# Kernel optimization log

Measured on AMD Instinct MI355X. Metric: run time of the kernel, lower is better.

The kernel has to match this reference:

```python
import jax, jax.numpy as jnp
import numpy as np

H = 1024  # lstm_hidden_dim
E = 1024  # embedding_size
T = 512   # seq_len
B = 128   # batch


def setup_inputs() -> dict:
    key = jax.random.key(0)
    k0, k1, k2, k3 = jax.random.split(key, 4)
    bound = 1.0 / np.sqrt(H)
    embeds = jax.random.normal(k0, (T, B, E), dtype=jnp.float32)
    # Stacked gate weights in order [g, i, f, o]; same math as 8 separate GEMMs.
    W_x = jax.random.uniform(k1, (E, 4 * H), jnp.float32, -bound, bound)
    W_h = jax.random.uniform(k2, (H, 4 * H), jnp.float32, -bound, bound)
    b = jax.random.uniform(k3, (4 * H,), jnp.float32, -bound, bound)
    b = b.at[2 * H:3 * H].add(1.0)  # forget-gate bias +1
    return {"embeds": embeds, "W_x": W_x, "W_h": W_h, "b": b}


def reference(embeds, W_x, W_h, b):
    Tn, Bn, _ = embeds.shape
    # Batch all input projections into one big GEMM (same math as per-step GEMMs).
    xproj = jnp.einsum('tbe,ef->tbf', embeds, W_x) + b  # [T, B, 4H]
    h0 = jnp.zeros((Bn, H), embeds.dtype)
    c0 = jnp.zeros((Bn, H), embeds.dtype)

    def step(carry, xp):
        h, c = carry
        z = xp + h @ W_h  # [B, 4H]
        g = jnp.tanh(z[:, :H])
        i = jax.nn.sigmoid(z[:, H:2 * H])
        f = jax.nn.sigmoid(z[:, 2 * H:3 * H])
        o = jax.nn.sigmoid(z[:, 3 * H:])
        c_new = g * i + c * f
        h_new = jnp.tanh(c_new) * o
        # Original module records h BEFORE the update at step t (h_prev).
        return (h_new, c_new), h

    _, h_total = jax.lax.scan(step, (h0, c0), xproj)
    return h_total  # [T, B, H], h_total[0] is zeros
```

## Files before the change

### kernel.cpp

```cpp
#include <hip/hip_runtime.h>
#include <hip/hip_bf16.h>

typedef __attribute__((ext_vector_type(8)))  short          bf16x8;
typedef __attribute__((ext_vector_type(4)))  float          f32x4;
typedef __attribute__((ext_vector_type(8)))  unsigned short us8;

__device__ __forceinline__ unsigned short f2b(float f) {
  union { __hip_bfloat16 h; unsigned short u; } v;
  v.h = __float2bfloat16(f);
  return v.u;
}
__device__ __forceinline__ float b2f(unsigned short u) {
  union { unsigned u; float f; } v; v.u = ((unsigned)u) << 16; return v.f;
}
__device__ __forceinline__ float sigf(float x) {
  return __builtin_amdgcn_rcpf(1.f + __expf(-x));
}
__device__ __forceinline__ float tanhf_(float x) {
  return 2.f * __builtin_amdgcn_rcpf(1.f + __expf(-2.f * x)) - 1.f;
}

__global__ __launch_bounds__(256) void conv_all(const float* __restrict__ embeds,
                                                const float* __restrict__ Wx,
                                                const float* __restrict__ Wh,
                                                unsigned short* __restrict__ ebf,
                                                unsigned short* __restrict__ wxf,
                                                unsigned short* __restrict__ whp) {
  const int b = blockIdx.x;
  if (b < 32768) {
    const int id = b * 256 + threadIdx.x;
    const int l  = id & 63;
    const int kt = (id >> 6) & 31;
    const int rt = id >> 11;
    const size_t src = ((size_t)(rt * 16 + (l & 15))) * 1024 + kt * 32 + (l >> 4) * 8;
    const float4 v0 = *(const float4*)(embeds + src);
    const float4 v1 = *(const float4*)(embeds + src + 4);
    us8 o;
    o[0]=f2b(v0.x); o[1]=f2b(v0.y); o[2]=f2b(v0.z); o[3]=f2b(v0.w);
    o[4]=f2b(v1.x); o[5]=f2b(v1.y); o[6]=f2b(v1.z); o[7]=f2b(v1.w);
    *(us8*)(ebf + (size_t)id * 8) = o;
  } else if (b < 34816) {
    const int id = (b - 32768) * 256 + threadIdx.x;
    const int l  = id & 63;
    const int kt = (id >> 6) & 31;
    const int c  = id >> 11;
    const int col = c * 16 + (l & 15);
    const int k0 = kt * 32 + (l >> 4) * 8;
    us8 o;
    #pragma unroll
    for (int j = 0; j < 8; ++j) o[j] = f2b(Wx[(size_t)(k0 + j) * 4096 + col]);
    *(us8*)(wxf + (size_t)id * 8) = o;
  } else {
    const int id = (b - 34816) * 256 + threadIdx.x;
    const int l  = id & 63;
    const int kt = (id >> 6) & 7;
    const int nt = (id >> 9) & 7;
    const int kq = (id >> 12) & 3;
    const int n  = id >> 14;
    const int zi = nt * 16 + (l & 15);
    const int col = (zi >> 5) * 1024 + n * 32 + (zi & 31);
    const int k0 = kq * 256 + kt * 32 + (l >> 4) * 8;
    us8 o;
    #pragma unroll
    for (int j = 0; j < 8; ++j) o[j] = f2b(Wh[(size_t)(k0 + j) * 4096 + col]);
    *(us8*)(whp + (size_t)id * 8) = o;
  }
}

__global__ __launch_bounds__(256, 2) void gemm_xproj_reg(
    const unsigned short* __restrict__ ebf,
    const unsigned short* __restrict__ wxf,
    const float* __restrict__ bias,
    unsigned short* __restrict__ xp) {
  const int lane = threadIdx.x & 63;
  const int wv = threadIdx.x >> 6;
  const int w = blockIdx.x * 4 + wv;
  const int ct = w & 31;
  const int rt = w >> 5;

  float bvf[8];
  #pragma unroll
  for (int nt = 0; nt < 8; ++nt) bvf[nt] = bias[ct * 128 + nt * 16 + (lane & 15)];

  f32x4 acc[4][8];
  #pragma unroll
  for (int a = 0; a < 4; ++a)
    #pragma unroll
    for (int nt = 0; nt < 8; ++nt) acc[a][nt] = f32x4{0.f,0.f,0.f,0.f};

  for (int kt = 0; kt < 32; ++kt) {
    bf16x8 af[4], bfr[8];
    #pragma unroll
    for (int a = 0; a < 4; ++a)
      af[a] = *(const bf16x8*)(ebf + (size_t)((4 * rt + a) * 32 + kt) * 512 + lane * 8);
    #pragma unroll
    for (int nt = 0; nt < 8; ++nt)
      bfr[nt] = *(const bf16x8*)(wxf + (size_t)((ct * 8 + nt) * 32 + kt) * 512 + lane * 8);
    #pragma unroll
    for (int a = 0; a < 4; ++a)
      #pragma unroll
      for (int nt = 0; nt < 8; ++nt)
        acc[a][nt] = __builtin_amdgcn_mfma_f32_16x16x32_bf16(af[a], bfr[nt], acc[a][nt], 0, 0, 0);
  }

  #pragma unroll
  for (int a = 0; a < 4; ++a) {
    const int row0 = rt * 64 + a * 16 + (lane >> 4) * 4;
    #pragma unroll
    for (int nt = 0; nt < 8; ++nt) {
      const int col = ct * 128 + nt * 16 + (lane & 15);
      #pragma unroll
      for (int rr = 0; rr < 4; ++rr)
        xp[(size_t)(row0 + rr) * 4096 + col] = f2b(acc[a][nt][rr] + bvf[nt]);
    }
  }
}

__global__ __launch_bounds__(256, 1) void lstm_recur(
    const unsigned short* __restrict__ xproj,
    const unsigned short* __restrict__ Wp,
    unsigned short* __restrict__ hbuf,
    float* __restrict__ out,
    unsigned* __restrict__ flags) {
  __shared__ float zpart[10][16][132];
  const int tid = threadIdx.x;
  const int lane = tid & 63;
  const int kq = tid >> 6;
  const int m = blockIdx.x >> 5;
  const int n = blockIdx.x & 31;

  bf16x8 wf[64];
  {
    const unsigned short* wb = Wp + ((size_t)(n * 4 + kq) * 64) * 512 + lane * 8;
    #pragma unroll
    for (int f = 0; f < 64; ++f) wf[f] = *(const bf16x8*)(wb + f * 512);
  }

  const int r    = tid >> 4;
  const int hg   = tid & 15;
  const int hc0  = n * 32 + hg * 2;
  const int grow = m * 16 + r;

  float cr0 = 0.f, cr1 = 0.f;
  const size_t xbase = (size_t)grow * 4096 + hc0;
  unsigned* bcast = flags + (m * 32 + (lane & 31)) * 32 + n;
  const unsigned* myf = flags + (size_t)(m * 32 + n) * 32 + kq * 8 + (lane & 7);

  unsigned xu0, xu1, xu2, xu3;
  {
    const unsigned short* xpp = xproj + xbase;
    asm volatile("global_load_dword %0, %1, off" : "=v"(xu0) : "v"(xpp));
    asm volatile("global_load_dword %0, %1, off" : "=v"(xu1) : "v"(xpp + 1024));
    asm volatile("global_load_dword %0, %1, off" : "=v"(xu2) : "v"(xpp + 2048));
    asm volatile("global_load_dword %0, %1, off" : "=v"(xu3) : "v"(xpp + 3072));
  }

  const size_t aoff = ((size_t)(m * 16 + (lane & 15))) * 1024 + kq * 256 + (lane >> 4) * 8;

  for (int t = 0; t < 511; ++t) {
    const unsigned short* ab = hbuf + (t & 1) * 131072 + aoff;

    bf16x8 av0, av1, av2, av3, av4, av5, av6, av7;
    __builtin_amdgcn_sched_barrier(0);
    asm volatile("global_load_dwordx4 %0, %1, off sc0 sc1"            : "=v"(av0) : "v"(ab));
    asm volatile("global_load_dwordx4 %0, %1, off offset:64 sc0 sc1"  : "=v"(av1) : "v"(ab));
    asm volatile("global_load_dwordx4 %0, %1, off offset:128 sc0 sc1" : "=v"(av2) : "v"(ab));
    asm volatile("global_load_dwordx4 %0, %1, off offset:192 sc0 sc1" : "=v"(av3) : "v"(ab));
    asm volatile("global_load_dwordx4 %0, %1, off offset:256 sc0 sc1" : "=v"(av4) : "v"(ab));
    asm volatile("global_load_dwordx4 %0, %1, off offset:320 sc0 sc1" : "=v"(av5) : "v"(ab));
    asm volatile("global_load_dwordx4 %0, %1, off offset:384 sc0 sc1" : "=v"(av6) : "v"(ab));
    asm volatile("global_load_dwordx4 %0, %1, off offset:448 sc0 sc1" : "=v"(av7) : "v"(ab));
    asm volatile("s_waitcnt vmcnt(0)" ::: "memory");
    __builtin_amdgcn_sched_barrier(0);

    f32x4 ac0 = {0.f,0.f,0.f,0.f}, ac1 = {0.f,0.f,0.f,0.f};
    f32x4 ac2 = {0.f,0.f,0.f,0.f}, ac3 = {0.f,0.f,0.f,0.f};
    f32x4 ac4 = {0.f,0.f,0.f,0.f}, ac5 = {0.f,0.f,0.f,0.f};
    f32x4 ac6 = {0.f,0.f,0.f,0.f}, ac7 = {0.f,0.f,0.f,0.f};
#define MF_STEP(AV, KT) \
    ac0 = __builtin_amdgcn_mfma_f32_16x16x32_bf16(AV, wf[ 0 + KT], ac0, 0, 0, 0); \
    ac1 = __builtin_amdgcn_mfma_f32_16x16x32_bf16(AV, wf[ 8 + KT], ac1, 0, 0, 0); \
    ac2 = __builtin_amdgcn_mfma_f32_16x16x32_bf16(AV, wf[16 + KT], ac2, 0, 0, 0); \
    ac3 = __builtin_amdgcn_mfma_f32_16x16x32_bf16(AV, wf[24 + KT], ac3, 0, 0, 0); \
    ac4 = __builtin_amdgcn_mfma_f32_16x16x32_bf16(AV, wf[32 + KT], ac4, 0, 0, 0); \
    ac5 = __builtin_amdgcn_mfma_f32_16x16x32_bf16(AV, wf[40 + KT], ac5, 0, 0, 0); \
    ac6 = __builtin_amdgcn_mfma_f32_16x16x32_bf16(AV, wf[48 + KT], ac6, 0, 0, 0); \
    ac7 = __builtin_amdgcn_mfma_f32_16x16x32_bf16(AV, wf[56 + KT], ac7, 0, 0, 0);
    MF_STEP(av0, 0) MF_STEP(av1, 1) MF_STEP(av2, 2) MF_STEP(av3, 3)
    MF_STEP(av4, 4) MF_STEP(av5, 5) MF_STEP(av6, 6) MF_STEP(av7, 7)
#undef MF_STEP

    {
      const int crow = (lane >> 4) * 4, ccol = lane & 15;
#define DUMP(NT, AC) \
      zpart[kq][crow + 0][NT * 16 + ccol] = AC[0]; \
      zpart[kq][crow + 1][NT * 16 + ccol] = AC[1]; \
      zpart[kq][crow + 2][NT * 16 + ccol] = AC[2]; \
      zpart[kq][crow + 3][NT * 16 + ccol] = AC[3];
      DUMP(0, ac0) DUMP(1, ac1) DUMP(2, ac2) DUMP(3, ac3)
      DUMP(4, ac4) DUMP(5, ac5) DUMP(6, ac6) DUMP(7, ac7)
#undef DUMP
    }
    __syncthreads();

    float zc[4][2];
    #pragma unroll
    for (int g = 0; g < 4; ++g)
      #pragma unroll
      for (int j = 0; j < 2; ++j) {
        const int col = g * 32 + hg * 2 + j;
        zc[g][j] = (zpart[0][r][col] + zpart[1][r][col])
                 + (zpart[2][r][col] + zpart[3][r][col]);
      }

    float hv0, hv1;
    {
      const float zg = zc[0][0] + b2f((unsigned short)(xu0 & 0xffffu));
      const float zi = zc[1][0] + b2f((unsigned short)(xu1 & 0xffffu));
      const float zf = zc[2][0] + b2f((unsigned short)(xu2 & 0xffffu));
      const float zo = zc[3][0] + b2f((unsigned short)(xu3 & 0xffffu));
      cr0 = tanhf_(zg) * sigf(zi) + cr0 * sigf(zf);
      hv0 = tanhf_(cr0) * sigf(zo);
    }
    {
      const float zg = zc[0][1] + b2f((unsigned short)(xu0 >> 16));
      const float zi = zc[1][1] + b2f((unsigned short)(xu1 >> 16));
      const float zf = zc[2][1] + b2f((unsigned short)(xu2 >> 16));
      const float zo = zc[3][1] + b2f((unsigned short)(xu3 >> 16));
      cr1 = tanhf_(zg) * sigf(zi) + cr1 * sigf(zf);
      hv1 = tanhf_(cr1) * sigf(zo);
    }

    if (t < 510) {
      const unsigned hp = (unsigned)f2b(hv0) | ((unsigned)f2b(hv1) << 16);
      unsigned short* hd = hbuf + ((t & 1) ^ 1) * 131072 + (size_t)grow * 1024 + hc0;
      asm volatile("global_store_dword %0, %1, off sc0 sc1" :: "v"(hd), "v"(hp) : "memory");
      asm volatile("s_waitcnt vmcnt(0)" ::: "memory");
      __syncthreads();
      if (kq == 0 && lane < 32) {
        const unsigned g1 = (unsigned)(t + 1);
        asm volatile("global_store_dword %0, %1, off sc0 sc1" :: "v"(bcast), "v"(g1) : "memory");
      }
    }

    float2 ho; ho.x = hv0; ho.y = hv1;
    *(float2*)(out + ((size_t)(t + 1) * 128 + grow) * 1024 + hc0) = ho;

    if (t < 510) {
      const unsigned short* xpp = xproj + (size_t)(t + 1) * 524288 + xbase;
      asm volatile("global_load_dword %0, %1, off" : "=v"(xu0) : "v"(xpp));
      asm volatile("global_load_dword %0, %1, off" : "=v"(xu1) : "v"(xpp + 1024));
      asm volatile("global_load_dword %0, %1, off" : "=v"(xu2) : "v"(xpp + 2048));
      asm volatile("global_load_dword %0, %1, off" : "=v"(xu3) : "v"(xpp + 3072));
      unsigned v;
      do {
        asm volatile("global_load_dword %0, %1, off sc0 sc1" : "=v"(v) : "v"(myf));
        asm volatile("s_waitcnt vmcnt(0)" ::: "memory");
      } while (__any((int)v <= t));
    }
  }
}

extern "C" void kernel_launch(void* const* d_in, const int* in_sizes, int n_in,
                              void* d_out, int out_size, void* d_ws, size_t ws_size,
                              hipStream_t stream) {
  (void)in_sizes; (void)n_in; (void)out_size; (void)ws_size;
  const float* embeds = (const float*)d_in[0];
  const float* Wx     = (const float*)d_in[1];
  const float* Wh     = (const float*)d_in[2];
  const float* bias   = (const float*)d_in[3];
  float* out = (float*)d_out;

  char* w = (char*)d_ws;
  unsigned short* ebf = (unsigned short*)(w);
  unsigned short* wxf = (unsigned short*)(w + 134217728);
  unsigned short* whp = (unsigned short*)(w + 142606336);
  unsigned short* xpb = (unsigned short*)(w + 150994944);
  unsigned short* hb  = (unsigned short*)(w + 687865856);
  unsigned*       fl  = (unsigned*)(w + 688390144);

  hipMemsetAsync(d_out, 0, (size_t)128 * 1024 * sizeof(float), stream);
  hipMemsetAsync(hb, 0, 524288, stream);
  hipMemsetAsync(fl, 0, 32768, stream);

  conv_all      <<<36864, 256, 0, stream>>>(embeds, Wx, Wh, ebf, wxf, whp);
  gemm_xproj_reg<<<8192,  256, 0, stream>>>(ebf, wxf, bias, xpb);
  lstm_recur    <<<256,   256, 0, stream>>>(xpb, whp, hb, out, fl);
}
```

Measured before the change: 2.829 ms.

## Replace register-only xproj GEMM with LDS double-buffered 256x256 tiled GEMM

```diff
diff --git a/kernel.cpp b/kernel.cpp
--- a/kernel.cpp
+++ b/kernel.cpp
@@ -23,35 +23,37 @@
 __global__ __launch_bounds__(256) void conv_all(const float* __restrict__ embeds,
                                                 const float* __restrict__ Wx,
                                                 const float* __restrict__ Wh,
-                                                unsigned short* __restrict__ ebf,
-                                                unsigned short* __restrict__ wxf,
+                                                unsigned short* __restrict__ eb,
+                                                unsigned short* __restrict__ WxT,
                                                 unsigned short* __restrict__ whp) {
+  __shared__ float tile[64][65];
   const int b = blockIdx.x;
   if (b < 32768) {
-    const int id = b * 256 + threadIdx.x;
-    const int l  = id & 63;
-    const int kt = (id >> 6) & 31;
-    const int rt = id >> 11;
-    const size_t src = ((size_t)(rt * 16 + (l & 15))) * 1024 + kt * 32 + (l >> 4) * 8;
-    const float4 v0 = *(const float4*)(embeds + src);
-    const float4 v1 = *(const float4*)(embeds + src + 4);
+    const size_t i = ((size_t)b * 256 + threadIdx.x) * 8;
+    const float4 v0 = *(const float4*)(embeds + i);
+    const float4 v1 = *(const float4*)(embeds + i + 4);
     us8 o;
     o[0]=f2b(v0.x); o[1]=f2b(v0.y); o[2]=f2b(v0.z); o[3]=f2b(v0.w);
     o[4]=f2b(v1.x); o[5]=f2b(v1.y); o[6]=f2b(v1.z); o[7]=f2b(v1.w);
-    *(us8*)(ebf + (size_t)id * 8) = o;
-  } else if (b < 34816) {
-    const int id = (b - 32768) * 256 + threadIdx.x;
-    const int l  = id & 63;
-    const int kt = (id >> 6) & 31;
-    const int c  = id >> 11;
-    const int col = c * 16 + (l & 15);
-    const int k0 = kt * 32 + (l >> 4) * 8;
-    us8 o;
-    #pragma unroll
-    for (int j = 0; j < 8; ++j) o[j] = f2b(Wx[(size_t)(k0 + j) * 4096 + col]);
-    *(us8*)(wxf + (size_t)id * 8) = o;
+    *(us8*)(eb + i) = o;
+  } else if (b < 33792) {
+    const int b2 = b - 32768;
+    const int bx = b2 & 63;
+    const int by = b2 >> 6;
+    const int tc = threadIdx.x & 63, tr = threadIdx.x >> 6;
+    #pragma unroll
+    for (int i = 0; i < 16; ++i) {
+      const int r = i * 4 + tr;
+      tile[r][tc] = Wx[(size_t)(by * 64 + r) * 4096 + bx * 64 + tc];
+    }
+    __syncthreads();
+    #pragma unroll
+    for (int i = 0; i < 16; ++i) {
+      const int c = i * 4 + tr;
+      WxT[(size_t)(bx * 64 + c) * 1024 + by * 64 + tc] = f2b(tile[tc][c]);
+    }
   } else {
-    const int id = (b - 34816) * 256 + threadIdx.x;
+    const int id = (b - 33792) * 256 + threadIdx.x;
     const int l  = id & 63;
     const int kt = (id >> 6) & 7;
     const int nt = (id >> 9) & 7;
@@ -67,51 +69,116 @@
   }
 }
 
-__global__ __launch_bounds__(256, 2) void gemm_xproj_reg(
-    const unsigned short* __restrict__ ebf,
-    const unsigned short* __restrict__ wxf,
+__global__ __launch_bounds__(512, 1) void gemm_xproj_8p(
+    const unsigned short* __restrict__ A,
+    const unsigned short* __restrict__ B,
     const float* __restrict__ bias,
-    unsigned short* __restrict__ xp) {
-  const int lane = threadIdx.x & 63;
-  const int wv = threadIdx.x >> 6;
-  const int w = blockIdx.x * 4 + wv;
-  const int ct = w & 31;
-  const int rt = w >> 5;
-
-  float bvf[8];
+    unsigned short* __restrict__ C) {
+  __shared__ unsigned short lds[2][2][2][8192];
+  const int tid = threadIdx.x;
+  const int lane = tid & 63;
+  const int wv = tid >> 6;
+  const int wr = wv >> 2;
+  const int wc = wv & 3;
+  const int sid = (blockIdx.x & 7) * 512 + (blockIdx.x >> 3);
+  const int bm = sid >> 4;
+  const int bn = sid & 15;
+  const int l15 = lane & 15;
+
+  const int kx0e = (((lane >> 4) * 16) ^ ((lane & 7) << 4)) >> 1;
+  const int kx1e = ((64 + (lane >> 4) * 16) ^ ((lane & 7) << 4)) >> 1;
+
+  const int srow0 = wv * 16 + (lane >> 3);
+  const int srow1 = wv * 16 + 8 + (lane >> 3);
+  const int skoff = 8 * ((lane & 7) ^ (lane >> 3));
+
+#define STAGE(D, MAT, HALF, GSRC, GROW0, KT2) { \
+    const unsigned short* s0_ = (GSRC) + (size_t)((GROW0) + srow0) * 1024 + (KT2) * 64 + skoff; \
+    const unsigned short* s1_ = (GSRC) + (size_t)((GROW0) + srow1) * 1024 + (KT2) * 64 + skoff; \
+    __builtin_amdgcn_global_load_lds( \
+        (const __attribute__((address_space(1))) unsigned short*)s0_, \
+        (__attribute__((address_space(3))) unsigned short*)(&lds[D][MAT][HALF][(wv * 2) * 512]), 16, 0, 0); \
+    __builtin_amdgcn_global_load_lds( \
+        (const __attribute__((address_space(1))) unsigned short*)s1_, \
+        (__attribute__((address_space(3))) unsigned short*)(&lds[D][MAT][HALF][(wv * 2 + 1) * 512]), 16, 0, 0); }
+
+  float bvf[4];
   #pragma unroll
-  for (int nt = 0; nt < 8; ++nt) bvf[nt] = bias[ct * 128 + nt * 16 + (lane & 15)];
-
-  f32x4 acc[4][8];
+  for (int nf = 0; nf < 4; ++nf)
+    bvf[nf] = bias[bn * 256 + wc * 64 + nf * 16 + l15];
+
+  f32x4 acc[8][4];
   #pragma unroll
-  for (int a = 0; a < 4; ++a)
-    #pragma unroll
-    for (int nt = 0; nt < 8; ++nt) acc[a][nt] = f32x4{0.f,0.f,0.f,0.f};
-
-  for (int kt = 0; kt < 32; ++kt) {
-    bf16x8 af[4], bfr[8];
-    #pragma unroll
-    for (int a = 0; a < 4; ++a)
-      af[a] = *(const bf16x8*)(ebf + (size_t)((4 * rt + a) * 32 + kt) * 512 + lane * 8);
-    #pragma unroll
-    for (int nt = 0; nt < 8; ++nt)
-      bfr[nt] = *(const bf16x8*)(wxf + (size_t)((ct * 8 + nt) * 32 + kt) * 512 + lane * 8);
-    #pragma unroll
-    for (int a = 0; a < 4; ++a)
+  for (int mf = 0; mf < 8; ++mf)
+    #pragma unroll
+    for (int nf = 0; nf < 4; ++nf) acc[mf][nf] = f32x4{0.f, 0.f, 0.f, 0.f};
+
+  STAGE(0, 0, 0, A, bm * 256, 0)
+  STAGE(0, 0, 1, A, bm * 256 + 128, 0)
+  STAGE(0, 1, 0, B, bn * 256, 0)
+  STAGE(0, 1, 1, B, bn * 256 + 128, 0)
+  asm volatile("s_waitcnt vmcnt(0)" ::: "memory");
+  __builtin_amdgcn_s_barrier();
+
+  for (int kt = 0; kt < 16; ++kt) {
+    const int cur = kt & 1;
+    bf16x8 bv[4][2];
+    #pragma unroll
+    for (int nf = 0; nf < 4; ++nf) {
+      const int brow = (wc & 1) * 64 + nf * 16 + l15;
+      bv[nf][0] = *(const bf16x8*)(&lds[cur][1][wc >> 1][brow * 64 + kx0e]);
+      bv[nf][1] = *(const bf16x8*)(&lds[cur][1][wc >> 1][brow * 64 + kx1e]);
+    }
+    #pragma unroll
+    for (int p = 0; p < 4; ++p) {
+      bf16x8 av[2][2];
       #pragma unroll
-      for (int nt = 0; nt < 8; ++nt)
-        acc[a][nt] = __builtin_amdgcn_mfma_f32_16x16x32_bf16(af[a], bfr[nt], acc[a][nt], 0, 0, 0);
-  }
+      for (int mf2 = 0; mf2 < 2; ++mf2) {
+        const int arow = (p * 2 + mf2) * 16 + l15;
+        av[mf2][0] = *(const bf16x8*)(&lds[cur][0][wr][arow * 64 + kx0e]);
+        av[mf2][1] = *(const bf16x8*)(&lds[cur][0][wr][arow * 64 + kx1e]);
+      }
+      if (kt < 15) {
+        if (p == 0) {
+          STAGE(cur ^ 1, 0, 0, A, bm * 256, kt + 1)
+          STAGE(cur ^ 1, 0, 1, A, bm * 256 + 128, kt + 1)
+        } else if (p == 1) {
+          STAGE(cur ^ 1, 1, 0, B, bn * 256, kt + 1)
+          STAGE(cur ^ 1, 1, 1, B, bn * 256 + 128, kt + 1)
+        }
+      }
+      if (p == 3 && kt < 15)
+        asm volatile("s_waitcnt vmcnt(0)" ::: "memory");
+      __builtin_amdgcn_sched_barrier(0);
+      __builtin_amdgcn_s_barrier();
+      asm volatile("s_waitcnt lgkmcnt(0)" ::: "memory");
+      __builtin_amdgcn_sched_barrier(0);
+      __builtin_amdgcn_s_setprio(1);
+      #pragma unroll
+      for (int mf2 = 0; mf2 < 2; ++mf2)
+        #pragma unroll
+        for (int nf = 0; nf < 4; ++nf) {
+          acc[p * 2 + mf2][nf] =
+              __builtin_amdgcn_mfma_f32_16x16x32_bf16(av[mf2][0], bv[nf][0], acc[p * 2 + mf2][nf], 0, 0, 0);
+          acc[p * 2 + mf2][nf] =
+              __builtin_amdgcn_mfma_f32_16x16x32_bf16(av[mf2][1], bv[nf][1], acc[p * 2 + mf2][nf], 0, 0, 0);
+        }
+      __builtin_amdgcn_s_setprio(0);
+      __builtin_amdgcn_sched_barrier(0);
+      __builtin_amdgcn_s_barrier();
+    }
+  }
+#undef STAGE
 
   #pragma unroll
-  for (int a = 0; a < 4; ++a) {
-    const int row0 = rt * 64 + a * 16 + (lane >> 4) * 4;
-    #pragma unroll
-    for (int nt = 0; nt < 8; ++nt) {
-      const int col = ct * 128 + nt * 16 + (lane & 15);
+  for (int mf = 0; mf < 8; ++mf) {
+    const int row0 = bm * 256 + wr * 128 + mf * 16 + (lane >> 4) * 4;
+    #pragma unroll
+    for (int nf = 0; nf < 4; ++nf) {
+      const int col = bn * 256 + wc * 64 + nf * 16 + l15;
       #pragma unroll
       for (int rr = 0; rr < 4; ++rr)
-        xp[(size_t)(row0 + rr) * 4096 + col] = f2b(acc[a][nt][rr] + bvf[nt]);
+        C[(size_t)(row0 + rr) * 4096 + col] = f2b(acc[mf][nf][rr] + bvf[nf]);
     }
   }
 }
@@ -272,8 +339,8 @@
   float* out = (float*)d_out;
 
   char* w = (char*)d_ws;
-  unsigned short* ebf = (unsigned short*)(w);
-  unsigned short* wxf = (unsigned short*)(w + 134217728);
+  unsigned short* eb  = (unsigned short*)(w);
+  unsigned short* WxT = (unsigned short*)(w + 134217728);
   unsigned short* whp = (unsigned short*)(w + 142606336);
   unsigned short* xpb = (unsigned short*)(w + 150994944);
   unsigned short* hb  = (unsigned short*)(w + 687865856);
@@ -283,7 +350,7 @@
   hipMemsetAsync(hb, 0, 524288, stream);
   hipMemsetAsync(fl, 0, 32768, stream);
 
-  conv_all      <<<36864, 256, 0, stream>>>(embeds, Wx, Wh, ebf, wxf, whp);
-  gemm_xproj_reg<<<8192,  256, 0, stream>>>(ebf, wxf, bias, xpb);
-  lstm_recur    <<<256,   256, 0, stream>>>(xpb, whp, hb, out, fl);
-}
+  conv_all     <<<35840, 256, 0, stream>>>(embeds, Wx, Wh, eb, WxT, whp);
+  gemm_xproj_8p<<<4096,  512, 0, stream>>>(eb, WxT, bias, xpb);
+  lstm_recur   <<<256,   256, 0, stream>>>(xpb, whp, hb, out, fl);
+}
```

New measurement: 2.551 ms. 9.8% less time.
